# Kernel optimization log

Measured on AMD Instinct MI355X. Metric: run time of the kernel, lower is better.

The kernel has to match this reference:

```python
import jax, jax.numpy as jnp
import numpy as np

EPS = 1e-5          # torch BatchNorm1d default eps
NEG_SLOPE = 0.01    # torch LeakyReLU default negative_slope


def _per_type(x, W1, b1, W2, b2, gamma, beta):
    # HeteroLinear layer 1: [N, d_in] @ [d_in, H] + [H]
    h = x @ W1 + b1
    # HeteroLinear layer 2: [N, H] @ [H, D] + [D]
    h = h @ W2 + b2
    # BatchNorm1d in training mode: batch stats, biased variance
    mean = jnp.mean(h, axis=0)
    var = jnp.mean(jnp.square(h - mean), axis=0)
    hn = (h - mean) * jax.lax.rsqrt(var + EPS) * gamma + beta
    # LeakyReLU
    return jnp.where(hn >= 0, hn, NEG_SLOPE * hn)


def setup_inputs() -> dict:
    key = jax.random.key(0)
    ks = jax.random.split(key, 8)
    N_USER, N_ITEM = 400000, 600000
    D_USER, D_ITEM = 64, 128
    H, D_OUT = 256, 128
    s = 0.05  # weight init scale
    return {
        "x_user": jax.random.normal(ks[0], (N_USER, D_USER), jnp.float32),
        "x_item": jax.random.normal(ks[1], (N_ITEM, D_ITEM), jnp.float32),
        "W1_user": jax.random.normal(ks[2], (D_USER, H), jnp.float32) * s,
        "b1_user": jnp.zeros((H,), jnp.float32),
        "W1_item": jax.random.normal(ks[3], (D_ITEM, H), jnp.float32) * s,
        "b1_item": jnp.zeros((H,), jnp.float32),
        "W2_user": jax.random.normal(ks[4], (H, D_OUT), jnp.float32) * s,
        "b2_user": jnp.zeros((D_OUT,), jnp.float32),
        "W2_item": jax.random.normal(ks[5], (H, D_OUT), jnp.float32) * s,
        "b2_item": jnp.zeros((D_OUT,), jnp.float32),
        "gamma_user": jnp.ones((D_OUT,), jnp.float32),
        "beta_user": jnp.zeros((D_OUT,), jnp.float32),
        "gamma_item": jnp.ones((D_OUT,), jnp.float32),
        "beta_item": jnp.zeros((D_OUT,), jnp.float32),
    }


def reference(x_user, x_item,
              W1_user, b1_user, W1_item, b1_item,
              W2_user, b2_user, W2_item, b2_item,
              gamma_user, beta_user, gamma_item, beta_item):
    out_user = _per_type(x_user, W1_user, b1_user, W2_user, b2_user, gamma_user, beta_user)
    out_item = _per_type(x_item, W1_item, b1_item, W2_item, b2_item, gamma_item, beta_item)
    return (out_user, out_item)
```

## Files before the change

### kernel.cpp

```cpp
#include <hip/hip_runtime.h>


typedef __attribute__((ext_vector_type(8))) short bf16x8;
typedef __attribute__((ext_vector_type(4))) float f32x4;

#define NBUF 128

#define WT_U_OFF    0
#define WT_I_OFF    4096
#define SUM_U_OFF   12288
#define SQ_U_OFF    (12288 + 1*NBUF*128)
#define SUM_I_OFF   (12288 + 2*NBUF*128)
#define SQ_I_OFF    (12288 + 3*NBUF*128)
#define SCALE_U_OFF (12288 + 4*NBUF*128)
#define SHIFT_U_OFF (SCALE_U_OFF + 128)
#define SCALE_I_OFF (SCALE_U_OFF + 256)
#define SHIFT_I_OFF (SCALE_U_OFF + 384)

__device__ inline unsigned short f2bf(float f) {
  union { float f; unsigned u; } v; v.f = f;
  return (unsigned short)((v.u + 0x7fffu + ((v.u >> 16) & 1u)) >> 16);
}

__global__ void fuse_zero_kernel(const float* __restrict__ W1u, const float* __restrict__ W2u,
                                 const float* __restrict__ W1i, const float* __restrict__ W2i,
                                 float* __restrict__ ws) {
  const int b = blockIdx.x;
  const int c = threadIdx.x;
  const int tid = b * 128 + c;
  for (int i = tid; i < 4 * NBUF * 128; i += 192 * 128) ws[SUM_U_OFF + i] = 0.f;

  const float* W1; const float* W2; int k; unsigned short* wt; int K;
  if (b < 64) { W1 = W1u; W2 = W2u; k = b;      wt = (unsigned short*)(ws + WT_U_OFF); K = 64; }
  else        { W1 = W1i; W2 = W2i; k = b - 64; wt = (unsigned short*)(ws + WT_I_OFF); K = 128; }
  float s = 0.f;
  for (int j = 0; j < 256; ++j) s += W1[k * 256 + j] * W2[j * 128 + c];
  wt[c * K + k] = f2bf(s);
}

__global__ void finalize_kernel(float* __restrict__ ws,
                                const float* __restrict__ gU, const float* __restrict__ bU,
                                const float* __restrict__ gI, const float* __restrict__ bI,
                                float invNu, float invNi) {
  const int typ = blockIdx.x;
  const int c = threadIdx.x;
  const float* sums = ws + (typ ? SUM_I_OFF : SUM_U_OFF);
  const float* sqs  = ws + (typ ? SQ_I_OFF  : SQ_U_OFF);
  const float invN  = typ ? invNi : invNu;
  float s = 0.f, q = 0.f;
  for (int b2 = 0; b2 < NBUF; ++b2) { s += sums[b2 * 128 + c]; q += sqs[b2 * 128 + c]; }
  const float mean = s * invN;
  const float var  = q * invN - mean * mean;
  const float* g  = typ ? gI : gU;
  const float* be = typ ? bI : bU;
  const float sc = g[c] * rsqrtf(var + 1e-5f);
  const float sh = be[c] - mean * sc;
  ws[(typ ? SCALE_I_OFF : SCALE_U_OFF) + c] = sc;
  ws[(typ ? SHIFT_I_OFF : SHIFT_U_OFF) + c] = sh;
}

template <int K, bool STATS>
__global__ __launch_bounds__(256) void hgemm_kernel(
    const float* __restrict__ x,
    const unsigned short* __restrict__ wt,
    float* __restrict__ sum_buf, float* __restrict__ sq_buf,
    const float* __restrict__ scale, const float* __restrict__ shift,
    float* __restrict__ out)
{
  constexpr int KP = K + 8;
  __shared__ __align__(16) unsigned short xs[64 * KP];
  __shared__ __align__(16) unsigned short wsh[128 * KP];
  __shared__ float bsum[128];
  __shared__ float bsq[128];

  const int tid = threadIdx.x;
  const long long row0 = (long long)blockIdx.x * 64;

  if (STATS && tid < 128) { bsum[tid] = 0.f; bsq[tid] = 0.f; }

  {
    const uint4* src = (const uint4*)wt;
    constexpr int CH = 128 * K / 8;
    for (int i = tid; i < CH; i += 256) {
      const int r = (i * 8) / K, cc = (i * 8) % K;
      *(uint4*)&wsh[r * KP + cc] = src[i];
    }
  }
  {
    const float4* src = (const float4*)(x + row0 * K);
    constexpr int CH = 64 * K / 4;
    for (int i = tid; i < CH; i += 256) {
      const float4 v = src[i];
      const int r = (i * 4) / K, cc = (i * 4) % K;
      ushort4 p;
      p.x = f2bf(v.x); p.y = f2bf(v.y); p.z = f2bf(v.z); p.w = f2bf(v.w);
      *(ushort4*)&xs[r * KP + cc] = p;
    }
  }
  __syncthreads();

  const int lane = tid & 63;
  const int wave = tid >> 6;
  const int l16  = lane & 15;
  const int quad = lane >> 4;
  const int arow = wave * 16 + l16;

  f32x4 acc[8];
#pragma unroll
  for (int t = 0; t < 8; ++t) acc[t] = (f32x4){0.f, 0.f, 0.f, 0.f};

#pragma unroll
  for (int k0 = 0; k0 < K; k0 += 32) {
    const bf16x8 a = *(const bf16x8*)&xs[arow * KP + k0 + quad * 8];
#pragma unroll
    for (int t = 0; t < 8; ++t) {
      const bf16x8 b = *(const bf16x8*)&wsh[(t * 16 + l16) * KP + k0 + quad * 8];
      acc[t] = __builtin_amdgcn_mfma_f32_16x16x32_bf16(a, b, acc[t], 0, 0, 0);
    }
  }

  if (STATS) {
#pragma unroll
    for (int t = 0; t < 8; ++t) {
      float s1 = acc[t][0] + acc[t][1] + acc[t][2] + acc[t][3];
      float s2 = acc[t][0] * acc[t][0] + acc[t][1] * acc[t][1] +
                 acc[t][2] * acc[t][2] + acc[t][3] * acc[t][3];
      s1 += __shfl_xor(s1, 16, 64);  s2 += __shfl_xor(s2, 16, 64);
      s1 += __shfl_xor(s1, 32, 64);  s2 += __shfl_xor(s2, 32, 64);
      if (quad == 0) {
        atomicAdd(&bsum[t * 16 + l16], s1);
        atomicAdd(&bsq[t * 16 + l16], s2);
      }
    }
    __syncthreads();
    if (tid < 128) {
      const int buf = blockIdx.x & (NBUF - 1);
      atomicAdd(&sum_buf[buf * 128 + tid], bsum[tid]);
      atomicAdd(&sq_buf[buf * 128 + tid], bsq[tid]);
    }
  } else {
#pragma unroll
    for (int t = 0; t < 8; ++t) {
      const int c = t * 16 + l16;
      const float sc = scale[c];
      const float sh = shift[c];
#pragma unroll
      for (int i = 0; i < 4; ++i) {
        const long long r = row0 + wave * 16 + quad * 4 + i;
        float v = acc[t][i] * sc + sh;
        v = (v >= 0.f) ? v : 0.01f * v;
        out[r * 128 + c] = v;
      }
    }
  }
}

extern "C" void kernel_launch(void* const* d_in, const int* in_sizes, int n_in,
                              void* d_out, int out_size, void* d_ws, size_t ws_size,
                              hipStream_t stream) {
  const float* xu  = (const float*)d_in[0];
  const float* xi  = (const float*)d_in[1];
  const float* W1u = (const float*)d_in[2];
  const float* W1i = (const float*)d_in[4];
  const float* W2u = (const float*)d_in[6];
  const float* W2i = (const float*)d_in[8];
  const float* gU  = (const float*)d_in[10];
  const float* bU  = (const float*)d_in[11];
  const float* gI  = (const float*)d_in[12];
  const float* bI  = (const float*)d_in[13];
  float* ws = (float*)d_ws;

  const int Nu = in_sizes[0] / 64;
  const int Ni = in_sizes[1] / 128;
  float* outU = (float*)d_out;
  float* outI = outU + (long long)Nu * 128;

  hipLaunchKernelGGL(fuse_zero_kernel, dim3(192), dim3(128), 0, stream,
                     W1u, W2u, W1i, W2i, ws);
  hipLaunchKernelGGL((hgemm_kernel<64, true>), dim3(Nu / 64), dim3(256), 0, stream,
                     xu, (const unsigned short*)(ws + WT_U_OFF),
                     ws + SUM_U_OFF, ws + SQ_U_OFF, nullptr, nullptr, nullptr);
  hipLaunchKernelGGL((hgemm_kernel<128, true>), dim3(Ni / 64), dim3(256), 0, stream,
                     xi, (const unsigned short*)(ws + WT_I_OFF),
                     ws + SUM_I_OFF, ws + SQ_I_OFF, nullptr, nullptr, nullptr);
  hipLaunchKernelGGL(finalize_kernel, dim3(2), dim3(128), 0, stream,
                     ws, gU, bU, gI, bI, 1.f / (float)Nu, 1.f / (float)Ni);
  hipLaunchKernelGGL((hgemm_kernel<64, false>), dim3(Nu / 64), dim3(256), 0, stream,
                     xu, (const unsigned short*)(ws + WT_U_OFF), nullptr, nullptr,
                     ws + SCALE_U_OFF, ws + SHIFT_U_OFF, outU);
  hipLaunchKernelGGL((hgemm_kernel<128, false>), dim3(Ni / 64), dim3(256), 0, stream,
                     xi, (const unsigned short*)(ws + WT_I_OFF), nullptr, nullptr,
                     ws + SCALE_I_OFF, ws + SHIFT_I_OFF, outI);
}
```

Baseline: 1.003 ms.

## Use persistent grid-stride waves with register-loaded inputs and fragment-packed weights

Replaces the one-block-per-64-rows GEMM with a fixed grid of 1024 persistent blocks, where each wave walks 16-row tiles in a grid-stride loop. Input rows are loaded straight from global memory into registers and converted to bf16 there, skipping the shared-memory staging. The fused weight is pre-packed into MFMA fragment order, so it is loaded into LDS once per block. BN statistics are accumulated in registers across tiles, which cuts the shared and global atomic traffic. The tradeoff is that the direct global loads for the A operand may coalesce less well, and there is less parallelism for hiding latency.

```diff
diff --git a/kernel.cpp b/kernel.cpp
--- a/kernel.cpp
+++ b/kernel.cpp
@@ -5,6 +5,7 @@
 typedef __attribute__((ext_vector_type(4))) float f32x4;
 
 #define NBUF 128
+#define GRID 1024
 
 #define WT_U_OFF    0
 #define WT_I_OFF    4096
@@ -22,6 +23,15 @@
   return (unsigned short)((v.u + 0x7fffu + ((v.u >> 16) & 1u)) >> 16);
 }
 
+__device__ inline bf16x8 cvt8(const float4 a, const float4 b) {
+  bf16x8 r;
+  r[0] = (short)f2bf(a.x); r[1] = (short)f2bf(a.y);
+  r[2] = (short)f2bf(a.z); r[3] = (short)f2bf(a.w);
+  r[4] = (short)f2bf(b.x); r[5] = (short)f2bf(b.y);
+  r[6] = (short)f2bf(b.z); r[7] = (short)f2bf(b.w);
+  return r;
+}
+
 __global__ void fuse_zero_kernel(const float* __restrict__ W1u, const float* __restrict__ W2u,
                                  const float* __restrict__ W1i, const float* __restrict__ W2i,
                                  float* __restrict__ ws) {
@@ -35,7 +45,10 @@
   else        { W1 = W1i; W2 = W2i; k = b - 64; wt = (unsigned short*)(ws + WT_I_OFF); K = 128; }
   float s = 0.f;
   for (int j = 0; j < 256; ++j) s += W1[k * 256 + j] * W2[j * 128 + c];
-  wt[c * K + k] = f2bf(s);
+  const int t = c >> 4, l16 = c & 15;
+  const int ks = k >> 5, quad = (k >> 3) & 3, j = k & 7;
+  const int f = t * (K / 32) + ks;
+  wt[(f * 64 + quad * 16 + l16) * 8 + j] = f2bf(s);
 }
 
 __global__ void finalize_kernel(float* __restrict__ ws,
@@ -65,66 +78,94 @@
     const unsigned short* __restrict__ wt,
     float* __restrict__ sum_buf, float* __restrict__ sq_buf,
     const float* __restrict__ scale, const float* __restrict__ shift,
-    float* __restrict__ out)
+    float* __restrict__ out,
+    int nTiles)
 {
-  constexpr int KP = K + 8;
-  __shared__ __align__(16) unsigned short xs[64 * KP];
-  __shared__ __align__(16) unsigned short wsh[128 * KP];
+  constexpr int NFRAG = 8 * (K / 32);
+  __shared__ __align__(16) unsigned short wsh[NFRAG * 64 * 8];
   __shared__ float bsum[128];
   __shared__ float bsq[128];
 
   const int tid = threadIdx.x;
-  const long long row0 = (long long)blockIdx.x * 64;
-
-  if (STATS && tid < 128) { bsum[tid] = 0.f; bsq[tid] = 0.f; }
 
   {
     const uint4* src = (const uint4*)wt;
-    constexpr int CH = 128 * K / 8;
-    for (int i = tid; i < CH; i += 256) {
-      const int r = (i * 8) / K, cc = (i * 8) % K;
-      *(uint4*)&wsh[r * KP + cc] = src[i];
-    }
-  }
-  {
-    const float4* src = (const float4*)(x + row0 * K);
-    constexpr int CH = 64 * K / 4;
-    for (int i = tid; i < CH; i += 256) {
-      const float4 v = src[i];
-      const int r = (i * 4) / K, cc = (i * 4) % K;
-      ushort4 p;
-      p.x = f2bf(v.x); p.y = f2bf(v.y); p.z = f2bf(v.z); p.w = f2bf(v.w);
-      *(ushort4*)&xs[r * KP + cc] = p;
-    }
-  }
+    uint4* dst = (uint4*)wsh;
+    constexpr int CH = NFRAG * 64;
+    for (int i = tid; i < CH; i += 256) dst[i] = src[i];
+  }
+  if (STATS && tid < 128) { bsum[tid] = 0.f; bsq[tid] = 0.f; }
   __syncthreads();
 
   const int lane = tid & 63;
   const int wave = tid >> 6;
   const int l16  = lane & 15;
   const int quad = lane >> 4;
-  const int arow = wave * 16 + l16;
-
-  f32x4 acc[8];
-#pragma unroll
-  for (int t = 0; t < 8; ++t) acc[t] = (f32x4){0.f, 0.f, 0.f, 0.f};
-
-#pragma unroll
-  for (int k0 = 0; k0 < K; k0 += 32) {
-    const bf16x8 a = *(const bf16x8*)&xs[arow * KP + k0 + quad * 8];
+  const unsigned short* wbase = &wsh[lane * 8];
+
+  float sc[8], sh[8];
+  if (!STATS) {
+#pragma unroll
+    for (int t = 0; t < 8; ++t) { sc[t] = scale[t * 16 + l16]; sh[t] = shift[t * 16 + l16]; }
+  }
+  float st1[8], st2[8];
+  if (STATS) {
+#pragma unroll
+    for (int t = 0; t < 8; ++t) { st1[t] = 0.f; st2[t] = 0.f; }
+  }
+
+  const int gwave   = blockIdx.x * 4 + wave;
+  const int wstride = gridDim.x * 4;
+
+  for (int tile = gwave; tile < nTiles; tile += wstride) {
+    const float* xr = x + (long long)(tile * 16 + l16) * K + quad * 8;
+    float4 af0[K / 32], af1[K / 32];
+#pragma unroll
+    for (int ks = 0; ks < K / 32; ++ks) {
+      af0[ks] = *(const float4*)(xr + ks * 32);
+      af1[ks] = *(const float4*)(xr + ks * 32 + 4);
+    }
+
+    f32x4 acc[8];
+#pragma unroll
+    for (int t = 0; t < 8; ++t) acc[t] = (f32x4){0.f, 0.f, 0.f, 0.f};
+
+#pragma unroll
+    for (int ks = 0; ks < K / 32; ++ks) {
+      const bf16x8 a = cvt8(af0[ks], af1[ks]);
+#pragma unroll
+      for (int t = 0; t < 8; ++t) {
+        const bf16x8 b = *(const bf16x8*)(wbase + (t * (K / 32) + ks) * 512);
+        acc[t] = __builtin_amdgcn_mfma_f32_16x16x32_bf16(a, b, acc[t], 0, 0, 0);
+      }
+    }
+
+    if (STATS) {
+#pragma unroll
+      for (int t = 0; t < 8; ++t) {
+        st1[t] += acc[t][0] + acc[t][1] + acc[t][2] + acc[t][3];
+        st2[t] += acc[t][0] * acc[t][0] + acc[t][1] * acc[t][1] +
+                  acc[t][2] * acc[t][2] + acc[t][3] * acc[t][3];
+      }
+    } else {
+#pragma unroll
+      for (int t = 0; t < 8; ++t) {
+        const int c = t * 16 + l16;
+#pragma unroll
+        for (int i = 0; i < 4; ++i) {
+          const long long r = (long long)tile * 16 + quad * 4 + i;
+          float v = acc[t][i] * sc[t] + sh[t];
+          v = (v >= 0.f) ? v : 0.01f * v;
+          out[r * 128 + c] = v;
+        }
+      }
+    }
+  }
+
+  if (STATS) {
 #pragma unroll
     for (int t = 0; t < 8; ++t) {
-      const bf16x8 b = *(const bf16x8*)&wsh[(t * 16 + l16) * KP + k0 + quad * 8];
-      acc[t] = __builtin_amdgcn_mfma_f32_16x16x32_bf16(a, b, acc[t], 0, 0, 0);
-    }
-  }
-
-  if (STATS) {
-#pragma unroll
-    for (int t = 0; t < 8; ++t) {
-      float s1 = acc[t][0] + acc[t][1] + acc[t][2] + acc[t][3];
-      float s2 = acc[t][0] * acc[t][0] + acc[t][1] * acc[t][1] +
-                 acc[t][2] * acc[t][2] + acc[t][3] * acc[t][3];
+      float s1 = st1[t], s2 = st2[t];
       s1 += __shfl_xor(s1, 16, 64);  s2 += __shfl_xor(s2, 16, 64);
       s1 += __shfl_xor(s1, 32, 64);  s2 += __shfl_xor(s2, 32, 64);
       if (quad == 0) {
@@ -137,20 +178,6 @@
       const int buf = blockIdx.x & (NBUF - 1);
       atomicAdd(&sum_buf[buf * 128 + tid], bsum[tid]);
       atomicAdd(&sq_buf[buf * 128 + tid], bsq[tid]);
-    }
-  } else {
-#pragma unroll
-    for (int t = 0; t < 8; ++t) {
-      const int c = t * 16 + l16;
-      const float sc = scale[c];
-      const float sh = shift[c];
-#pragma unroll
-      for (int i = 0; i < 4; ++i) {
-        const long long r = row0 + wave * 16 + quad * 4 + i;
-        float v = acc[t][i] * sc + sh;
-        v = (v >= 0.f) ? v : 0.01f * v;
-        out[r * 128 + c] = v;
-      }
     }
   }
 }
@@ -177,18 +204,18 @@
 
   hipLaunchKernelGGL(fuse_zero_kernel, dim3(192), dim3(128), 0, stream,
                      W1u, W2u, W1i, W2i, ws);
-  hipLaunchKernelGGL((hgemm_kernel<64, true>), dim3(Nu / 64), dim3(256), 0, stream,
+  hipLaunchKernelGGL((hgemm_kernel<64, true>), dim3(GRID), dim3(256), 0, stream,
                      xu, (const unsigned short*)(ws + WT_U_OFF),
-                     ws + SUM_U_OFF, ws + SQ_U_OFF, nullptr, nullptr, nullptr);
-  hipLaunchKernelGGL((hgemm_kernel<128, true>), dim3(Ni / 64), dim3(256), 0, stream,
+                     ws + SUM_U_OFF, ws + SQ_U_OFF, nullptr, nullptr, nullptr, Nu / 16);
+  hipLaunchKernelGGL((hgemm_kernel<128, true>), dim3(GRID), dim3(256), 0, stream,
                      xi, (const unsigned short*)(ws + WT_I_OFF),
-                     ws + SUM_I_OFF, ws + SQ_I_OFF, nullptr, nullptr, nullptr);
+                     ws + SUM_I_OFF, ws + SQ_I_OFF, nullptr, nullptr, nullptr, Ni / 16);
   hipLaunchKernelGGL(finalize_kernel, dim3(2), dim3(128), 0, stream,
                      ws, gU, bU, gI, bI, 1.f / (float)Nu, 1.f / (float)Ni);
-  hipLaunchKernelGGL((hgemm_kernel<64, false>), dim3(Nu / 64), dim3(256), 0, stream,
+  hipLaunchKernelGGL((hgemm_kernel<64, false>), dim3(GRID), dim3(256), 0, stream,
                      xu, (const unsigned short*)(ws + WT_U_OFF), nullptr, nullptr,
-                     ws + SCALE_U_OFF, ws + SHIFT_U_OFF, outU);
-  hipLaunchKernelGGL((hgemm_kernel<128, false>), dim3(Ni / 64), dim3(256), 0, stream,
+                     ws + SCALE_U_OFF, ws + SHIFT_U_OFF, outU, Nu / 16);
+  hipLaunchKernelGGL((hgemm_kernel<128, false>), dim3(GRID), dim3(256), 0, stream,
                      xi, (const unsigned short*)(ws + WT_I_OFF), nullptr, nullptr,
-                     ws + SCALE_I_OFF, ws + SHIFT_I_OFF, outI);
-}
+                     ws + SCALE_I_OFF, ws + SHIFT_I_OFF, outI, Ni / 16);
+}
```

Result: faster. 939.1 us (-6.4%).
